# Optimization experiments

Hardware: AMD Instinct MI355X
Metric: run time of the kernel (lower is better)

Reference implementation:

```python
import jax, jax.numpy as jnp
import numpy as np

EPS_BN = 1e-5
NEG_SLOPE = 0.2

def gat_layer(x, src, dst, N, W, a_src, a_dst, b, heads, ch, concat):
    # x: [N, Fin]; W: [Fin, heads*ch]; a_src/a_dst: [heads, ch]; b: [heads*ch] or [ch]
    xw = (x @ W).reshape(N, heads, ch)                      # [N,H,C]
    al_src = jnp.einsum('nhc,hc->nh', xw, a_src)            # [N,H]
    al_dst = jnp.einsum('nhc,hc->nh', xw, a_dst)
    e = jax.nn.leaky_relu(al_src[src] + al_dst[dst], NEG_SLOPE)  # [E,H]
    m = jax.ops.segment_max(e, dst, num_segments=N)         # segment softmax (stable)
    ee = jnp.exp(e - m[dst])
    s = jax.ops.segment_sum(ee, dst, num_segments=N)
    alpha = ee / (s[dst] + 1e-16)                            # [E,H]
    msg = xw[src] * alpha[:, :, None]                        # [E,H,C]
    out = jax.ops.segment_sum(msg, dst, num_segments=N)      # [N,H,C]
    if concat:
        return out.reshape(N, heads * ch) + b
    return out.mean(axis=1) + b

def setup_inputs():
    key = jax.random.key(0)
    ks = jax.random.split(key, 24)
    N, E, dim_in, dim_out = 20000, 320000, 256, 16
    x = jax.random.normal(ks[0], (N, dim_in), dtype=jnp.float32)
    edge_index = jax.random.randint(ks[1], (2, E), 0, N, dtype=jnp.int64)
    def glorot(k, shape):
        fan = shape[0] + shape[-1]
        return jax.random.uniform(k, shape, jnp.float32, -1.0, 1.0) * np.sqrt(6.0 / fan)
    return {
        'x': x, 'edge_index': edge_index,
        'bn_gamma': jnp.ones((dim_in,), jnp.float32),
        'bn_beta': jnp.zeros((dim_in,), jnp.float32),
        'W1': glorot(ks[2], (dim_in, 16 * 64)),
        'a1_src': glorot(ks[3], (16, 64)), 'a1_dst': glorot(ks[4], (16, 64)),
        'b1': jnp.zeros((16 * 64,), jnp.float32),
        'p1': jnp.float32(0.25),
        'W2': glorot(ks[5], (dim_in + 16 * 64, 8 * 8)),
        'a2_src': glorot(ks[6], (8, 8)), 'a2_dst': glorot(ks[7], (8, 8)),
        'b2': jnp.zeros((8 * 8,), jnp.float32),
        'p2': jnp.float32(0.25),
        'W3': glorot(ks[8], (8 * 8, 8 * dim_out)),
        'a3_src': glorot(ks[9], (8, dim_out)), 'a3_dst': glorot(ks[10], (8, dim_out)),
        'b3': jnp.zeros((dim_out,), jnp.float32),
    }

def reference(x, edge_index, bn_gamma, bn_beta, W1, a1_src, a1_dst, b1, p1,
              W2, a2_src, a2_dst, b2, p2, W3, a3_src, a3_dst, b3):
    N = x.shape[0]
    # PyG GATConv default add_self_loops=True
    loops = jnp.arange(N, dtype=edge_index.dtype)
    src = jnp.concatenate([edge_index[0], loops])
    dst = jnp.concatenate([edge_index[1], loops])
    # BatchNorm1d (training-mode batch stats)
    mu = x.mean(axis=0)
    var = x.var(axis=0)
    x_in = (x - mu) * jax.lax.rsqrt(var + EPS_BN) * bn_gamma + bn_beta
    h = gat_layer(x_in, src, dst, N, W1, a1_src, a1_dst, b1, 16, 64, True)
    h = jnp.where(h >= 0, h, p1 * h)  # PReLU
    h = gat_layer(jnp.concatenate([x_in, h], axis=1), src, dst, N, W2, a2_src, a2_dst, b2, 8, 8, True)
    h = jnp.where(h >= 0, h, p2 * h)
    h = gat_layer(h, src, dst, N, W3, a3_src, a3_dst, b3, 8, b3.shape[0], False)
    return jax.nn.log_softmax(h, axis=1)
```

## Files before the change

### kernel.cpp

```cpp
#include <hip/hip_runtime.h>
#include <math.h>

typedef unsigned int u32;
typedef unsigned short u16;
typedef u32 u32x4 __attribute__((ext_vector_type(4)));
typedef float f32x4 __attribute__((ext_vector_type(4)));

__device__ __forceinline__ u16 f2bf(float f) {
  u32 u = __builtin_bit_cast(u32, f);
  return (u16)((u + 0x7FFFu + ((u >> 16) & 1u)) >> 16);
}
__device__ __forceinline__ float bf2f(u32 lo16) {
  return __builtin_bit_cast(float, lo16 << 16);
}
__device__ __forceinline__ void mfma16(f32x4& c, const u32x4& a, const u32x4& b) {
  asm volatile("v_mfma_f32_16x16x32_bf16 %0, %1, %2, %0" : "+v"(c) : "v"(a), "v"(b));
}
__device__ __forceinline__ float lrelu(float e) { return fmaxf(e, 0.2f * e); }

__global__ void bn_stats_kernel(const float* __restrict__ x, float* __restrict__ musum,
                                float* __restrict__ sqsum, int N, int F) {
  int t = threadIdx.x;
  float s = 0.f, s2 = 0.f;
  for (int r = blockIdx.x; r < N; r += gridDim.x) {
    float v = x[(size_t)r * F + t];
    s += v;
    s2 += v * v;
  }
  atomicAdd(&musum[t], s);
  atomicAdd(&sqsum[t], s2);
}

__global__ void bn_finalize_kernel(const float* __restrict__ musum, const float* __restrict__ sqsum,
                                   const float* __restrict__ gamma, const float* __restrict__ beta,
                                   float* __restrict__ scale, float* __restrict__ shift, int N) {
  int t = threadIdx.x;
  float m = musum[t] / (float)N;
  float v = sqsum[t] / (float)N - m * m;
  float sc = gamma[t] * rsqrtf(v + 1e-5f);
  scale[t] = sc;
  shift[t] = beta[t] - m * sc;
}

__global__ void bn_apply_bf16_kernel(const float* __restrict__ x, const float* __restrict__ scale,
                                     const float* __restrict__ shift, u16* __restrict__ xin,
                                     int total, int Fmask) {
  int i = blockIdx.x * blockDim.x + threadIdx.x;
  if (i < total) {
    int c = i & Fmask;
    xin[i] = f2bf(x[i] * scale[c] + shift[c]);
  }
}

__global__ void csr_count_kernel(const int* __restrict__ ei, int E, int N, int* __restrict__ cnt) {
  int e = blockIdx.x * blockDim.x + threadIdx.x;
  int ET = E + N;
  if (e < ET) {
    int d = (e < E) ? ei[E + e] : (e - E);
    atomicAdd(&cnt[d], 1);
  }
}

__global__ __launch_bounds__(1024) void csr_scan_kernel(const int* __restrict__ cnt,
                                                        int* __restrict__ row_ptr,
                                                        int* __restrict__ cursor, int N) {
  __shared__ int part[1024];
  int t = threadIdx.x;
  int chunk = (N + 1023) / 1024;
  int lo = t * chunk;
  int hi = min(lo + chunk, N);
  int s = 0;
  for (int i = lo; i < hi; i++) s += cnt[i];
  part[t] = s;
  __syncthreads();
  for (int off = 1; off < 1024; off <<= 1) {
    int v = (t >= off) ? part[t - off] : 0;
    __syncthreads();
    part[t] += v;
    __syncthreads();
  }
  int run = (t == 0) ? 0 : part[t - 1];
  for (int i = lo; i < hi; i++) {
    row_ptr[i] = run;
    cursor[i] = run;
    run += cnt[i];
  }
  if (t == 1023) row_ptr[N] = part[1023];
}

__global__ void csr_fill_kernel(const int* __restrict__ ei, int E, int N,
                                int* __restrict__ cursor, int* __restrict__ csr_src) {
  int e = blockIdx.x * blockDim.x + threadIdx.x;
  int ET = E + N;
  if (e < ET) {
    int s, d;
    if (e < E) { s = ei[e]; d = ei[E + e]; }
    else       { s = e - E; d = s; }
    int pos = atomicAdd(&cursor[d], 1);
    csr_src[pos] = s;
  }
}

__global__ __launch_bounds__(1024) void perm_build_kernel(const int* __restrict__ row_ptr,
                                                          int* __restrict__ perm, int N) {
  __shared__ int bins[256];
  __shared__ int base[256];
  int t = threadIdx.x;
  if (t < 256) bins[t] = 0;
  __syncthreads();
  for (int i = t; i < N; i += 1024) {
    int d = min(row_ptr[i + 1] - row_ptr[i], 255);
    atomicAdd(&bins[d], 1);
  }
  __syncthreads();
  for (int off = 1; off < 256; off <<= 1) {
    int u = (t < 256 && t >= off) ? bins[t - off] : 0;
    __syncthreads();
    if (t < 256) bins[t] += u;
    __syncthreads();
  }
  if (t < 256) base[t] = (t == 0) ? 0 : bins[t - 1];
  __syncthreads();
  if (t < 256) bins[t] = base[t];
  __syncthreads();
  for (int i = t; i < N; i += 1024) {
    int d = min(row_ptr[i + 1] - row_ptr[i], 255);
    int pos = atomicAdd(&bins[d], 1);
    perm[pos] = i;
  }
}

__global__ void wt_build_all(const float* __restrict__ W1, const float* __restrict__ W2,
                             const float* __restrict__ W3, u16* __restrict__ Wt1,
                             u16* __restrict__ Wt2, u16* __restrict__ Wt3) {
  const int S1 = 1024 * 256, S2 = 64 * 1280, S3 = 128 * 64;
  const int P1 = 96 * 256, P2 = 32 * 1280, P3 = 32 * 64;
  int idx = blockIdx.x * blockDim.x + threadIdx.x;
  if (idx < S1) {
    int n = idx / 256, k = idx % 256;
    Wt1[idx] = f2bf(W1[(size_t)k * 1024 + n]);
  } else if (idx < S1 + S2) {
    int i = idx - S1;
    int n = i / 1280, k = i % 1280;
    Wt2[i] = f2bf(W2[(size_t)k * 64 + n]);
  } else if (idx < S1 + S2 + S3) {
    int i = idx - S1 - S2;
    int n = i / 64, k = i % 64;
    Wt3[i] = f2bf(W3[(size_t)k * 128 + n]);
  } else if (idx < S1 + S2 + S3 + P1) {
    Wt1[S1 + (idx - S1 - S2 - S3)] = 0;
  } else if (idx < S1 + S2 + S3 + P1 + P2) {
    Wt2[S2 + (idx - S1 - S2 - S3 - P1)] = 0;
  } else if (idx < S1 + S2 + S3 + P1 + P2 + P3) {
    Wt3[S3 + (idx - S1 - S2 - S3 - P1 - P2)] = 0;
  }
}

__global__ void alfold_build(const float* __restrict__ W1, const float* __restrict__ a1s,
                             const float* __restrict__ a1d, const float* __restrict__ W2,
                             const float* __restrict__ a2s, const float* __restrict__ a2d,
                             const float* __restrict__ W3, const float* __restrict__ a3s,
                             const float* __restrict__ a3d, u16* __restrict__ Wt1,
                             u16* __restrict__ Wt2, u16* __restrict__ Wt3) {
  const int T1 = 32 * 256, T2 = 16 * 1280, T3 = 16 * 64;
  int idx = blockIdx.x * blockDim.x + threadIdx.x;
  if (idx < T1) {
    int jj = idx / 256, k = idx % 256, h = jj >> 1;
    const float* av = (jj & 1) ? a1d : a1s;
    float s = 0.f;
    for (int c = 0; c < 64; c++) s += W1[(size_t)k * 1024 + h * 64 + c] * av[h * 64 + c];
    Wt1[(size_t)(1024 + jj) * 256 + k] = f2bf(s);
  } else if (idx < T1 + T2) {
    int i = idx - T1;
    int jj = i / 1280, k = i % 1280, h = jj >> 1;
    const float* av = (jj & 1) ? a2d : a2s;
    float s = 0.f;
    for (int c = 0; c < 8; c++) s += W2[(size_t)k * 64 + h * 8 + c] * av[h * 8 + c];
    Wt2[(size_t)(64 + jj) * 1280 + k] = f2bf(s);
  } else if (idx < T1 + T2 + T3) {
    int i = idx - T1 - T2;
    int jj = i / 64, k = i % 64, h = jj >> 1;
    const float* av = (jj & 1) ? a3d : a3s;
    float s = 0.f;
    for (int c = 0; c < 16; c++) s += W3[(size_t)k * 128 + h * 16 + c] * av[h * 16 + c];
    Wt3[(size_t)(128 + jj) * 64 + k] = f2bf(s);
  }
}

template <int BM, int BN, int FM, int FN>
__global__ __launch_bounds__(256) void mfma_gemm_al(
    const u16* __restrict__ A1, const u16* __restrict__ A2, int K1, int K,
    const u16* __restrict__ Wt, u16* __restrict__ Ch, int NcH,
    float* __restrict__ als, float* __restrict__ ald, int ALN, int ALP, int M) {
  constexpr int BK = 32;
  constexpr int ACH = (BM * BK) / 8;
  constexpr int BCH = (BN * BK) / 8;
  static_assert(BM == 2 * FM * 16 && BN == 2 * FN * 16, "wave grid 2x2");
  __shared__ u16 As[BM * BK];
  __shared__ u16 Bs[BN * BK];
  int t = threadIdx.x;
  int m0 = blockIdx.x * BM, n0 = blockIdx.y * BN;
  int r = t & 15;
  int g = (t >> 4) & 3;
  int wid = t >> 6;
  int wm0 = (wid >> 1) * (FM * 16);
  int wn0 = (wid & 1) * (FN * 16);
  int K8 = K >> 3;
  int K2 = K - K1;

  f32x4 acc[FM][FN] = {};
  asm volatile("s_nop 7\n\ts_nop 7" :::);

  for (int k0 = 0; k0 < K; k0 += BK) {
    const u16* Aseg;
    int sA, kl;
    if (k0 < K1) { Aseg = A1; sA = K1; kl = k0; }
    else         { Aseg = A2; sA = K2; kl = k0 - K1; }
    __syncthreads();
#pragma unroll
    for (int i = 0; i < (ACH + 255) / 256; i++) {
      int c = i * 256 + t;
      if (ACH % 256 == 0 || c < ACH) {
        int m = c >> 2, kb = c & 3;
        *(u32x4*)(As + c * 8) =
            *(const u32x4*)(Aseg + (size_t)(m0 + m) * sA + kl + kb * 8);
      }
    }
#pragma unroll
    for (int i = 0; i < (BCH + 255) / 256; i++) {
      int c = i * 256 + t;
      if (BCH % 256 == 0 || c < BCH) {
        int nn = c >> 2, kb = c & 3;
        *(u32x4*)(Bs + c * 8) =
            *(const u32x4*)(Wt + ((size_t)(n0 + nn) * K8 + (k0 >> 3) + kb) * 8);
      }
    }
    __syncthreads();
    u32x4 af[FM], bfr[FN];
#pragma unroll
    for (int fi = 0; fi < FM; fi++)
      af[fi] = *(const u32x4*)(As + ((wm0 + fi * 16 + r) * 4 + g) * 8);
#pragma unroll
    for (int fj = 0; fj < FN; fj++)
      bfr[fj] = *(const u32x4*)(Bs + ((wn0 + fj * 16 + r) * 4 + g) * 8);
#pragma unroll
    for (int fi = 0; fi < FM; fi++)
#pragma unroll
      for (int fj = 0; fj < FN; fj++) mfma16(acc[fi][fj], af[fi], bfr[fj]);
  }
  asm volatile("s_nop 7\n\ts_nop 7" :::);

#pragma unroll
  for (int fi = 0; fi < FM; fi++) {
#pragma unroll
    for (int fj = 0; fj < FN; fj++) {
#pragma unroll
      for (int v = 0; v < 4; v++) {
        int m = m0 + wm0 + fi * 16 + g * 4 + v;
        int nn = n0 + wn0 + fj * 16 + r;
        if (m < M) {
          float val = acc[fi][fj][v];
          if (nn < NcH) {
            Ch[(size_t)m * NcH + nn] = f2bf(val);
          } else {
            int j = nn - NcH;
            if (j < ALN) ((j & 1) ? ald : als)[(size_t)(j >> 1) * ALP + m] = val;
          }
        }
      }
    }
  }
}

__global__ __launch_bounds__(256) void gat_agg1_gs(
    const u16* __restrict__ xwh, const float* __restrict__ alsrc,
    const float* __restrict__ aldst, const int* __restrict__ row_ptr,
    const int* __restrict__ csr_src, const int* __restrict__ perm,
    const float* __restrict__ bias, const float* __restrict__ slope_p,
    u16* __restrict__ out, int N, int ALP, int NBH) {
  constexpr int U = 4;
  int b = blockIdx.x;
  int xcd = b & 7, seq = b >> 3;
  int phase = seq / NBH, nb = seq - phase * NBH;
  int h = xcd + (phase << 3);
  int lane = threadIdx.x & 63;
  int g = lane >> 3, l8 = lane & 7;
  int ti = nb * 32 + (threadIdx.x >> 6) * 8 + g;
  int n = perm[min(ti, N - 1)];
  const float* alh = alsrc + (size_t)h * ALP;
  float ad = aldst[(size_t)h * ALP + n];
  int start = row_ptr[n];
  int end = row_ptr[n + 1];
  int deg = (ti < N) ? end - start : 0;
  int endm1 = end - 1;

  float m = -1e30f, s = 0.f;
  float acc[8] = {};
  const u16* base = xwh + (size_t)h * 64 + (size_t)l8 * 8;

  auto fma8 = [&](const u32x4& v, float w) {
#pragma unroll
    for (int i = 0; i < 4; i++) {
      u32 u = v[i];
      acc[2 * i] = fmaf(w, bf2f(u & 0xffffu), acc[2 * i]);
      acc[2 * i + 1] = fmaf(w, bf2f(u >> 16), acc[2 * i + 1]);
    }
  };

  int c[U];
#pragma unroll
  for (int i = 0; i < U; i++) c[i] = csr_src[min(start + i, endm1)];
  int j = 0;
  for (; j + U <= deg; j += U) {
    u32x4 v[U];
    float e[U];
#pragma unroll
    for (int i = 0; i < U; i++) v[i] = *(const u32x4*)(base + (size_t)c[i] * 1024);
#pragma unroll
    for (int i = 0; i < U; i++) e[i] = lrelu(alh[c[i]] + ad);
#pragma unroll
    for (int i = 0; i < U; i++) c[i] = csr_src[min(start + j + U + i, endm1)];
    float mn = fmaxf(fmaxf(e[0], e[1]), fmaxf(e[2], e[3]));
    if (mn > m) {
      float sc = __expf(m - mn);
      s *= sc;
#pragma unroll
      for (int k = 0; k < 8; k++) acc[k] *= sc;
      m = mn;
    }
#pragma unroll
    for (int i = 0; i < U; i++) {
      float w = __expf(e[i] - m);
      s += w;
      fma8(v[i], w);
    }
  }
  for (int i = 0; j < deg; j++, i++) {
    u32x4 v = *(const u32x4*)(base + (size_t)c[i] * 1024);
    float e = lrelu(alh[c[i]] + ad);
    if (e > m) {
      float sc = __expf(m - e);
      s *= sc;
#pragma unroll
      for (int k = 0; k < 8; k++) acc[k] *= sc;
      m = e;
    }
    float w = __expf(e - m);
    s += w;
    fma8(v, w);
  }
  float rr = 1.f / (s + 1e-16f);

  if (ti < N) {
    float p = slope_p[0];
    u32 ow[4];
#pragma unroll
    for (int i = 0; i < 4; i++) {
      int cc = h * 64 + l8 * 8 + 2 * i;
      float v0 = acc[2 * i] * rr + bias[cc];
      float v1 = acc[2 * i + 1] * rr + bias[cc + 1];
      v0 = (v0 >= 0.f) ? v0 : p * v0;
      v1 = (v1 >= 0.f) ? v1 : p * v1;
      ow[i] = (u32)f2bf(v0) | ((u32)f2bf(v1) << 16);
    }
    *(u32x4*)(out + (size_t)n * 1024 + h * 64 + l8 * 8) = *(u32x4*)ow;
  }
}

__global__ __launch_bounds__(256) void gat_agg2_wave(
    const u16* __restrict__ xwh, const float* __restrict__ alsrc,
    const float* __restrict__ aldst, const int* __restrict__ row_ptr,
    const int* __restrict__ csr_src, const float* __restrict__ bias,
    const float* __restrict__ slope_p, u16* __restrict__ out, int N, int ALP) {
  constexpr int U = 8;
  int n = blockIdx.x * 4 + (threadIdx.x >> 6);
  if (n >= N) return;
  int lane = threadIdx.x & 63;
  int head = lane >> 3;
  const float* alh = alsrc + (size_t)head * ALP;
  float ad = aldst[(size_t)head * ALP + n];
  int start = row_ptr[n];
  int end = row_ptr[n + 1];
  int deg = end - start;
  int endm1 = end - 1;

  float m = -1e30f, s = 0.f, acc = 0.f;
  int c[U];
#pragma unroll
  for (int i = 0; i < U; i++) c[i] = csr_src[min(start + i, endm1)];
  int j = 0;
  for (; j + U <= deg; j += U) {
    u16 v[U];
    float e[U];
#pragma unroll
    for (int i = 0; i < U; i++) v[i] = xwh[(size_t)c[i] * 64 + lane];
#pragma unroll
    for (int i = 0; i < U; i++) e[i] = lrelu(alh[c[i]] + ad);
#pragma unroll
    for (int i = 0; i < U; i++) c[i] = csr_src[min(start + j + U + i, endm1)];
    float mn = e[0];
#pragma unroll
    for (int i = 1; i < U; i++) mn = fmaxf(mn, e[i]);
    if (mn > m) {
      float sc = __expf(m - mn);
      s *= sc;
      acc *= sc;
      m = mn;
    }
#pragma unroll
    for (int i = 0; i < U; i++) {
      float w = __expf(e[i] - m);
      s += w;
      acc = fmaf(w, bf2f(v[i]), acc);
    }
  }
  for (int i = 0; j < deg; j++, i++) {
    float vv = bf2f(xwh[(size_t)c[i] * 64 + lane]);
    float e = lrelu(alh[c[i]] + ad);
    if (e > m) {
      float sc = __expf(m - e);
      s *= sc;
      acc *= sc;
      m = e;
    }
    float w = __expf(e - m);
    s += w;
    acc = fmaf(w, vv, acc);
  }
  float rr = 1.f / (s + 1e-16f);

  float p = slope_p[0];
  float v = acc * rr + bias[lane];
  out[(size_t)n * 64 + lane] = f2bf((v >= 0.f) ? v : p * v);
}

__global__ __launch_bounds__(256) void gat_agg3_wave(
    const u16* __restrict__ xwh, const float* __restrict__ alsrc,
    const float* __restrict__ aldst, const int* __restrict__ row_ptr,
    const int* __restrict__ csr_src, const float* __restrict__ bias,
    float* __restrict__ out, int N, int ALP) {
  constexpr int U = 8;
  int n = blockIdx.x * 4 + (threadIdx.x >> 6);
  if (n >= N) return;
  int lane = threadIdx.x & 63;
  int head = lane >> 3;
  const float* alh = alsrc + (size_t)head * ALP;
  float ad = aldst[(size_t)head * ALP + n];
  int start = row_ptr[n];
  int end = row_ptr[n + 1];
  int deg = end - start;
  int endm1 = end - 1;

  float m = -1e30f, s = 0.f, a0 = 0.f, a1 = 0.f;
  int c[U];
#pragma unroll
  for (int i = 0; i < U; i++) c[i] = csr_src[min(start + i, endm1)];
  int j = 0;
  for (; j + U <= deg; j += U) {
    u32 v[U];
    float e[U];
#pragma unroll
    for (int i = 0; i < U; i++) v[i] = *(const u32*)(xwh + (size_t)c[i] * 128 + lane * 2);
#pragma unroll
    for (int i = 0; i < U; i++) e[i] = lrelu(alh[c[i]] + ad);
#pragma unroll
    for (int i = 0; i < U; i++) c[i] = csr_src[min(start + j + U + i, endm1)];
    float mn = e[0];
#pragma unroll
    for (int i = 1; i < U; i++) mn = fmaxf(mn, e[i]);
    if (mn > m) {
      float sc = __expf(m - mn);
      s *= sc;
      a0 *= sc;
      a1 *= sc;
      m = mn;
    }
#pragma unroll
    for (int i = 0; i < U; i++) {
      float w = __expf(e[i] - m);
      s += w;
      a0 = fmaf(w, bf2f(v[i] & 0xffffu), a0);
      a1 = fmaf(w, bf2f(v[i] >> 16), a1);
    }
  }
  for (int i = 0; j < deg; j++, i++) {
    u32 v = *(const u32*)(xwh + (size_t)c[i] * 128 + lane * 2);
    float e = lrelu(alh[c[i]] + ad);
    if (e > m) {
      float sc = __expf(m - e);
      s *= sc;
      a0 *= sc;
      a1 *= sc;
      m = e;
    }
    float w = __expf(e - m);
    s += w;
    a0 = fmaf(w, bf2f(v & 0xffffu), a0);
    a1 = fmaf(w, bf2f(v >> 16), a1);
  }
  float rr = 1.f / (s + 1e-16f);
  a0 *= rr;
  a1 *= rr;

#pragma unroll
  for (int st = 8; st <= 32; st <<= 1) {
    a0 += __shfl_xor(a0, st);
    a1 += __shfl_xor(a1, st);
  }
  int c0 = (2 * lane) & 15, c1 = (2 * lane + 1) & 15;
  float v0 = a0 * 0.125f + bias[c0];
  float v1 = a1 * 0.125f + bias[c1];
  float mx = fmaxf(v0, v1);
#pragma unroll
  for (int st = 1; st <= 4; st <<= 1) mx = fmaxf(mx, __shfl_xor(mx, st));
  float se = __expf(v0 - mx) + __expf(v1 - mx);
#pragma unroll
  for (int st = 1; st <= 4; st <<= 1) se += __shfl_xor(se, st);
  float lse = mx + logf(se);
  if (lane < 8) {
    float2 o = make_float2(v0 - lse, v1 - lse);
    *((float2*)(out + (size_t)n * 16) + lane) = o;
  }
}

extern "C" void kernel_launch(void* const* d_in, const int* in_sizes, int n_in,
                              void* d_out, int out_size, void* d_ws, size_t ws_size,
                              hipStream_t stream) {
  const float* x        = (const float*)d_in[0];
  const int*   ei       = (const int*)d_in[1];
  const float* bn_gamma = (const float*)d_in[2];
  const float* bn_beta  = (const float*)d_in[3];
  const float* W1       = (const float*)d_in[4];
  const float* a1s      = (const float*)d_in[5];
  const float* a1d      = (const float*)d_in[6];
  const float* b1       = (const float*)d_in[7];
  const float* p1       = (const float*)d_in[8];
  const float* W2       = (const float*)d_in[9];
  const float* a2s      = (const float*)d_in[10];
  const float* a2d      = (const float*)d_in[11];
  const float* b2       = (const float*)d_in[12];
  const float* p2       = (const float*)d_in[13];
  const float* W3       = (const float*)d_in[14];
  const float* a3s      = (const float*)d_in[15];
  const float* a3d      = (const float*)d_in[16];
  const float* b3       = (const float*)d_in[17];
  float* out = (float*)d_out;

  const int F  = in_sizes[2];
  const int N  = in_sizes[0] / F;
  const int E  = in_sizes[1] / 2;
  const int ET = E + N;
  const int MP = ((N + 127) / 128) * 128;

  size_t off = 0;
  auto alloc = [&](size_t bytes) -> char* {
    char* r = (char*)d_ws + off;
    off += (bytes + 255) & ~(size_t)255;
    return r;
  };
  float* musum   = (float*)alloc(F * 4);
  float* sqsum   = (float*)alloc(F * 4);
  float* scale   = (float*)alloc(F * 4);
  float* shift   = (float*)alloc(F * 4);
  int*   row_ptr = (int*)alloc((size_t)(N + 1) * 4);
  int*   cursor  = (int*)alloc((size_t)N * 4);
  int*   csr_src = (int*)alloc((size_t)ET * 4);
  int*   perm    = (int*)alloc((size_t)N * 4);
  float* al_s    = (float*)alloc((size_t)16 * MP * 4);
  float* al_d    = (float*)alloc((size_t)16 * MP * 4);
  u16*   Wt1     = (u16*)alloc((size_t)1152 * 256 * 2);
  u16*   Wt2     = (u16*)alloc((size_t)96 * 1280 * 2);
  u16*   Wt3     = (u16*)alloc((size_t)160 * 64 * 2);
  u16*   x_in_h  = (u16*)alloc((size_t)MP * 256 * 2);
  u16*   xw1h    = (u16*)alloc((size_t)MP * 1024 * 2);
  u16*   h1      = (u16*)alloc((size_t)MP * 1024 * 2);
  u16*   xw2h    = (u16*)alloc((size_t)MP * 64 * 2);
  u16*   h2h     = (u16*)alloc((size_t)MP * 64 * 2);
  u16*   xw3h    = (u16*)alloc((size_t)MP * 128 * 2);

  hipMemsetAsync(musum, 0, (size_t)2 * F * 4, stream);
  bn_stats_kernel<<<256, 256, 0, stream>>>(x, musum, sqsum, N, F);
  bn_finalize_kernel<<<1, F, 0, stream>>>(musum, sqsum, bn_gamma, bn_beta, scale, shift, N);
  int totalXF = N * F;
  bn_apply_bf16_kernel<<<(totalXF + 255) / 256, 256, 0, stream>>>(x, scale, shift, x_in_h,
                                                                  totalXF, F - 1);

  hipMemsetAsync(cursor, 0, (size_t)N * 4, stream);
  csr_count_kernel<<<(ET + 255) / 256, 256, 0, stream>>>(ei, E, N, cursor);
  csr_scan_kernel<<<1, 1024, 0, stream>>>(cursor, row_ptr, cursor, N);
  csr_fill_kernel<<<(ET + 255) / 256, 256, 0, stream>>>(ei, E, N, cursor, csr_src);

  perm_build_kernel<<<1, 1024, 0, stream>>>(row_ptr, perm, N);

  {
    int total = 1024 * 256 + 64 * 1280 + 128 * 64 + 96 * 256 + 32 * 1280 + 32 * 64;
    wt_build_all<<<(total + 255) / 256, 256, 0, stream>>>(W1, W2, W3, Wt1, Wt2, Wt3);
    int tot2 = 32 * 256 + 16 * 1280 + 16 * 64;
    alfold_build<<<(tot2 + 255) / 256, 256, 0, stream>>>(W1, a1s, a1d, W2, a2s, a2d, W3, a3s, a3d,
                                                         Wt1, Wt2, Wt3);
  }

  int nblk = (N + 3) / 4;

  {
    dim3 grid(MP / 128, 9);
    mfma_gemm_al<128, 128, 4, 4><<<grid, 256, 0, stream>>>(
        x_in_h, x_in_h, 256, 256, Wt1, xw1h, 1024, al_s, al_d, 32, MP, N);
    int NBH = (N + 31) / 32;
    gat_agg1_gs<<<8 * NBH * 2, 256, 0, stream>>>(xw1h, al_s, al_d, row_ptr, csr_src, perm, b1, p1,
                                                 h1, N, MP, NBH);
  }

  {
    dim3 grid((N + 63) / 64, 1);
    mfma_gemm_al<64, 96, 2, 3><<<grid, 256, 0, stream>>>(
        x_in_h, h1, 256, 1280, Wt2, xw2h, 64, al_s, al_d, 16, MP, N);
    gat_agg2_wave<<<nblk, 256, 0, stream>>>(xw2h, al_s, al_d, row_ptr, csr_src, b2, p2, h2h, N, MP);
  }

  {
    dim3 grid((N + 63) / 64, 1);
    mfma_gemm_al<64, 160, 2, 5><<<grid, 256, 0, stream>>>(
        h2h, h2h, 64, 64, Wt3, xw3h, 128, al_s, al_d, 16, MP, N);
    gat_agg3_wave<<<nblk, 256, 0, stream>>>(xw3h, al_s, al_d, row_ptr, csr_src, b3, out, N, MP);
  }
}
```

Baseline: 327.1 us.

## Double-buffer GEMM with direct global-to-LDS loads; regroup layer 2/3 aggregation lanes

```diff
diff --git a/kernel.cpp b/kernel.cpp
--- a/kernel.cpp
+++ b/kernel.cpp
@@ -196,8 +196,8 @@
   constexpr int ACH = (BM * BK) / 8;
   constexpr int BCH = (BN * BK) / 8;
   static_assert(BM == 2 * FM * 16 && BN == 2 * FN * 16, "wave grid 2x2");
-  __shared__ u16 As[BM * BK];
-  __shared__ u16 Bs[BN * BK];
+  __shared__ u16 As[2][BM * BK];
+  __shared__ u16 Bs[2][BN * BK];
   int t = threadIdx.x;
   int m0 = blockIdx.x * BM, n0 = blockIdx.y * BN;
   int r = t & 15;
@@ -208,22 +208,19 @@
   int K8 = K >> 3;
   int K2 = K - K1;
 
-  f32x4 acc[FM][FN] = {};
-  asm volatile("s_nop 7\n\ts_nop 7" :::);
-
-  for (int k0 = 0; k0 < K; k0 += BK) {
+  auto stage = [&](int buf, int k0) {
     const u16* Aseg;
     int sA, kl;
     if (k0 < K1) { Aseg = A1; sA = K1; kl = k0; }
     else         { Aseg = A2; sA = K2; kl = k0 - K1; }
-    __syncthreads();
 #pragma unroll
     for (int i = 0; i < (ACH + 255) / 256; i++) {
       int c = i * 256 + t;
       if (ACH % 256 == 0 || c < ACH) {
         int m = c >> 2, kb = c & 3;
-        *(u32x4*)(As + c * 8) =
-            *(const u32x4*)(Aseg + (size_t)(m0 + m) * sA + kl + kb * 8);
+        __builtin_amdgcn_global_load_lds(
+            (const __attribute__((address_space(1))) void*)(Aseg + (size_t)(m0 + m) * sA + kl + kb * 8),
+            (__attribute__((address_space(3))) void*)(&As[buf][c * 8]), 16, 0, 0);
       }
     }
 #pragma unroll
@@ -231,22 +228,34 @@
       int c = i * 256 + t;
       if (BCH % 256 == 0 || c < BCH) {
         int nn = c >> 2, kb = c & 3;
-        *(u32x4*)(Bs + c * 8) =
-            *(const u32x4*)(Wt + ((size_t)(n0 + nn) * K8 + (k0 >> 3) + kb) * 8);
+        __builtin_amdgcn_global_load_lds(
+            (const __attribute__((address_space(1))) void*)(Wt + ((size_t)(n0 + nn) * K8 + (k0 >> 3) + kb) * 8),
+            (__attribute__((address_space(3))) void*)(&Bs[buf][c * 8]), 16, 0, 0);
       }
     }
+  };
+
+  f32x4 acc[FM][FN] = {};
+  asm volatile("s_nop 7\n\ts_nop 7" :::);
+
+  stage(0, 0);
+  __syncthreads();
+  int nt = K / BK;
+  for (int ts = 0; ts < nt; ts++) {
+    if (ts + 1 < nt) stage((ts + 1) & 1, (ts + 1) * BK);
+    int cur = ts & 1;
+    u32x4 af[FM], bfr[FN];
+#pragma unroll
+    for (int fi = 0; fi < FM; fi++)
+      af[fi] = *(const u32x4*)(&As[cur][((wm0 + fi * 16 + r) * 4 + g) * 8]);
+#pragma unroll
+    for (int fj = 0; fj < FN; fj++)
+      bfr[fj] = *(const u32x4*)(&Bs[cur][((wn0 + fj * 16 + r) * 4 + g) * 8]);
+#pragma unroll
+    for (int fi = 0; fi < FM; fi++)
+#pragma unroll
+      for (int fj = 0; fj < FN; fj++) mfma16(acc[fi][fj], af[fi], bfr[fj]);
     __syncthreads();
-    u32x4 af[FM], bfr[FN];
-#pragma unroll
-    for (int fi = 0; fi < FM; fi++)
-      af[fi] = *(const u32x4*)(As + ((wm0 + fi * 16 + r) * 4 + g) * 8);
-#pragma unroll
-    for (int fj = 0; fj < FN; fj++)
-      bfr[fj] = *(const u32x4*)(Bs + ((wn0 + fj * 16 + r) * 4 + g) * 8);
-#pragma unroll
-    for (int fi = 0; fi < FM; fi++)
-#pragma unroll
-      for (int fj = 0; fj < FN; fj++) mfma16(acc[fi][fj], af[fi], bfr[fj]);
   }
   asm volatile("s_nop 7\n\ts_nop 7" :::);
 
@@ -367,159 +376,199 @@
   }
 }
 
-__global__ __launch_bounds__(256) void gat_agg2_wave(
+__global__ __launch_bounds__(256) void gat_agg2_gs(
     const u16* __restrict__ xwh, const float* __restrict__ alsrc,
     const float* __restrict__ aldst, const int* __restrict__ row_ptr,
-    const int* __restrict__ csr_src, const float* __restrict__ bias,
-    const float* __restrict__ slope_p, u16* __restrict__ out, int N, int ALP) {
-  constexpr int U = 8;
-  int n = blockIdx.x * 4 + (threadIdx.x >> 6);
-  if (n >= N) return;
+    const int* __restrict__ csr_src, const int* __restrict__ perm,
+    const float* __restrict__ bias, const float* __restrict__ slope_p,
+    u16* __restrict__ out, int N, int ALP) {
+  constexpr int U = 4;
   int lane = threadIdx.x & 63;
-  int head = lane >> 3;
+  int g = lane >> 3, l8 = lane & 7;
+  int ti = blockIdx.x * 32 + (threadIdx.x >> 6) * 8 + g;
+  int n = perm[min(ti, N - 1)];
+  const float* alh = alsrc + (size_t)l8 * ALP;
+  float ad = aldst[(size_t)l8 * ALP + n];
+  int start = row_ptr[n];
+  int end = row_ptr[n + 1];
+  int deg = (ti < N) ? end - start : 0;
+  int endm1 = end - 1;
+
+  float m = -1e30f, s = 0.f;
+  float acc[8] = {};
+  const u16* base = xwh + (size_t)l8 * 8;
+
+  auto fma8 = [&](const u32x4& v, float w) {
+#pragma unroll
+    for (int i = 0; i < 4; i++) {
+      u32 u = v[i];
+      acc[2 * i] = fmaf(w, bf2f(u & 0xffffu), acc[2 * i]);
+      acc[2 * i + 1] = fmaf(w, bf2f(u >> 16), acc[2 * i + 1]);
+    }
+  };
+
+  int c[U];
+#pragma unroll
+  for (int i = 0; i < U; i++) c[i] = csr_src[min(start + i, endm1)];
+  int j = 0;
+  for (; j + U <= deg; j += U) {
+    u32x4 v[U];
+    float e[U];
+#pragma unroll
+    for (int i = 0; i < U; i++) v[i] = *(const u32x4*)(base + (size_t)c[i] * 64);
+#pragma unroll
+    for (int i = 0; i < U; i++) e[i] = lrelu(alh[c[i]] + ad);
+#pragma unroll
+    for (int i = 0; i < U; i++) c[i] = csr_src[min(start + j + U + i, endm1)];
+    float mn = fmaxf(fmaxf(e[0], e[1]), fmaxf(e[2], e[3]));
+    if (mn > m) {
+      float sc = __expf(m - mn);
+      s *= sc;
+#pragma unroll
+      for (int k = 0; k < 8; k++) acc[k] *= sc;
+      m = mn;
+    }
+#pragma unroll
+    for (int i = 0; i < U; i++) {
+      float w = __expf(e[i] - m);
+      s += w;
+      fma8(v[i], w);
+    }
+  }
+  for (int i = 0; j < deg; j++, i++) {
+    u32x4 v = *(const u32x4*)(base + (size_t)c[i] * 64);
+    float e = lrelu(alh[c[i]] + ad);
+    if (e > m) {
+      float sc = __expf(m - e);
+      s *= sc;
+#pragma unroll
+      for (int k = 0; k < 8; k++) acc[k] *= sc;
+      m = e;
+    }
+    float w = __expf(e - m);
+    s += w;
+    fma8(v, w);
+  }
+  float rr = 1.f / (s + 1e-16f);
+
+  if (ti < N) {
+    float p = slope_p[0];
+    u32 ow[4];
+#pragma unroll
+    for (int i = 0; i < 4; i++) {
+      int cc = l8 * 8 + 2 * i;
+      float v0 = acc[2 * i] * rr + bias[cc];
+      float v1 = acc[2 * i + 1] * rr + bias[cc + 1];
+      v0 = (v0 >= 0.f) ? v0 : p * v0;
+      v1 = (v1 >= 0.f) ? v1 : p * v1;
+      ow[i] = (u32)f2bf(v0) | ((u32)f2bf(v1) << 16);
+    }
+    *(u32x4*)(out + (size_t)n * 64 + l8 * 8) = *(u32x4*)ow;
+  }
+}
+
+__global__ __launch_bounds__(256) void gat_agg3_gs(
+    const u16* __restrict__ xwh, const float* __restrict__ alsrc,
+    const float* __restrict__ aldst, const int* __restrict__ row_ptr,
+    const int* __restrict__ csr_src, const int* __restrict__ perm,
+    const float* __restrict__ bias, float* __restrict__ out, int N, int ALP) {
+  constexpr int U = 4;
+  int lane = threadIdx.x & 63;
+  int g = lane >> 4, l16 = lane & 15;
+  int head = l16 >> 1;
+  int ti = blockIdx.x * 16 + (threadIdx.x >> 6) * 4 + g;
+  int n = perm[min(ti, N - 1)];
   const float* alh = alsrc + (size_t)head * ALP;
   float ad = aldst[(size_t)head * ALP + n];
   int start = row_ptr[n];
   int end = row_ptr[n + 1];
-  int deg = end - start;
+  int deg = (ti < N) ? end - start : 0;
   int endm1 = end - 1;
 
-  float m = -1e30f, s = 0.f, acc = 0.f;
+  float m = -1e30f, s = 0.f;
+  float acc[8] = {};
+  const u16* base = xwh + (size_t)l16 * 8;
+
+  auto fma8 = [&](const u32x4& v, float w) {
+#pragma unroll
+    for (int i = 0; i < 4; i++) {
+      u32 u = v[i];
+      acc[2 * i] = fmaf(w, bf2f(u & 0xffffu), acc[2 * i]);
+      acc[2 * i + 1] = fmaf(w, bf2f(u >> 16), acc[2 * i + 1]);
+    }
+  };
+
   int c[U];
 #pragma unroll
   for (int i = 0; i < U; i++) c[i] = csr_src[min(start + i, endm1)];
   int j = 0;
   for (; j + U <= deg; j += U) {
-    u16 v[U];
+    u32x4 v[U];
     float e[U];
 #pragma unroll
-    for (int i = 0; i < U; i++) v[i] = xwh[(size_t)c[i] * 64 + lane];
+    for (int i = 0; i < U; i++) v[i] = *(const u32x4*)(base + (size_t)c[i] * 128);
 #pragma unroll
     for (int i = 0; i < U; i++) e[i] = lrelu(alh[c[i]] + ad);
 #pragma unroll
     for (int i = 0; i < U; i++) c[i] = csr_src[min(start + j + U + i, endm1)];
-    float mn = e[0];
-#pragma unroll
-    for (int i = 1; i < U; i++) mn = fmaxf(mn, e[i]);
+    float mn = fmaxf(fmaxf(e[0], e[1]), fmaxf(e[2], e[3]));
     if (mn > m) {
       float sc = __expf(m - mn);
       s *= sc;
-      acc *= sc;
+#pragma unroll
+      for (int k = 0; k < 8; k++) acc[k] *= sc;
       m = mn;
     }
 #pragma unroll
     for (int i = 0; i < U; i++) {
       float w = __expf(e[i] - m);
       s += w;
-      acc = fmaf(w, bf2f(v[i]), acc);
+      fma8(v[i], w);
     }
   }
   for (int i = 0; j < deg; j++, i++) {
-    float vv = bf2f(xwh[(size_t)c[i] * 64 + lane]);
+    u32x4 v = *(const u32x4*)(base + (size_t)c[i] * 128);
     float e = lrelu(alh[c[i]] + ad);
     if (e > m) {
       float sc = __expf(m - e);
       s *= sc;
-      acc *= sc;
+#pragma unroll
+      for (int k = 0; k < 8; k++) acc[k] *= sc;
       m = e;
     }
     float w = __expf(e - m);
     s += w;
-    acc = fmaf(w, vv, acc);
+    fma8(v, w);
   }
   float rr = 1.f / (s + 1e-16f);
-
-  float p = slope_p[0];
-  float v = acc * rr + bias[lane];
-  out[(size_t)n * 64 + lane] = f2bf((v >= 0.f) ? v : p * v);
-}
-
-__global__ __launch_bounds__(256) void gat_agg3_wave(
-    const u16* __restrict__ xwh, const float* __restrict__ alsrc,
-    const float* __restrict__ aldst, const int* __restrict__ row_ptr,
-    const int* __restrict__ csr_src, const float* __restrict__ bias,
-    float* __restrict__ out, int N, int ALP) {
-  constexpr int U = 8;
-  int n = blockIdx.x * 4 + (threadIdx.x >> 6);
-  if (n >= N) return;
-  int lane = threadIdx.x & 63;
-  int head = lane >> 3;
-  const float* alh = alsrc + (size_t)head * ALP;
-  float ad = aldst[(size_t)head * ALP + n];
-  int start = row_ptr[n];
-  int end = row_ptr[n + 1];
-  int deg = end - start;
-  int endm1 = end - 1;
-
-  float m = -1e30f, s = 0.f, a0 = 0.f, a1 = 0.f;
-  int c[U];
-#pragma unroll
-  for (int i = 0; i < U; i++) c[i] = csr_src[min(start + i, endm1)];
-  int j = 0;
-  for (; j + U <= deg; j += U) {
-    u32 v[U];
-    float e[U];
-#pragma unroll
-    for (int i = 0; i < U; i++) v[i] = *(const u32*)(xwh + (size_t)c[i] * 128 + lane * 2);
-#pragma unroll
-    for (int i = 0; i < U; i++) e[i] = lrelu(alh[c[i]] + ad);
-#pragma unroll
-    for (int i = 0; i < U; i++) c[i] = csr_src[min(start + j + U + i, endm1)];
-    float mn = e[0];
-#pragma unroll
-    for (int i = 1; i < U; i++) mn = fmaxf(mn, e[i]);
-    if (mn > m) {
-      float sc = __expf(m - mn);
-      s *= sc;
-      a0 *= sc;
-      a1 *= sc;
-      m = mn;
-    }
-#pragma unroll
-    for (int i = 0; i < U; i++) {
-      float w = __expf(e[i] - m);
-      s += w;
-      a0 = fmaf(w, bf2f(v[i] & 0xffffu), a0);
-      a1 = fmaf(w, bf2f(v[i] >> 16), a1);
-    }
-  }
-  for (int i = 0; j < deg; j++, i++) {
-    u32 v = *(const u32*)(xwh + (size_t)c[i] * 128 + lane * 2);
-    float e = lrelu(alh[c[i]] + ad);
-    if (e > m) {
-      float sc = __expf(m - e);
-      s *= sc;
-      a0 *= sc;
-      a1 *= sc;
-      m = e;
-    }
-    float w = __expf(e - m);
-    s += w;
-    a0 = fmaf(w, bf2f(v & 0xffffu), a0);
-    a1 = fmaf(w, bf2f(v >> 16), a1);
-  }
-  float rr = 1.f / (s + 1e-16f);
-  a0 *= rr;
-  a1 *= rr;
-
-#pragma unroll
-  for (int st = 8; st <= 32; st <<= 1) {
-    a0 += __shfl_xor(a0, st);
-    a1 += __shfl_xor(a1, st);
-  }
-  int c0 = (2 * lane) & 15, c1 = (2 * lane + 1) & 15;
-  float v0 = a0 * 0.125f + bias[c0];
-  float v1 = a1 * 0.125f + bias[c1];
-  float mx = fmaxf(v0, v1);
-#pragma unroll
-  for (int st = 1; st <= 4; st <<= 1) mx = fmaxf(mx, __shfl_xor(mx, st));
-  float se = __expf(v0 - mx) + __expf(v1 - mx);
-#pragma unroll
-  for (int st = 1; st <= 4; st <<= 1) se += __shfl_xor(se, st);
+#pragma unroll
+  for (int k = 0; k < 8; k++) acc[k] *= rr;
+
+#pragma unroll
+  for (int st = 2; st <= 8; st <<= 1)
+#pragma unroll
+    for (int k = 0; k < 8; k++) acc[k] += __shfl_xor(acc[k], st);
+
+  int half = l16 & 1;
+  float v8[8];
+  float mx = -1e30f;
+#pragma unroll
+  for (int k = 0; k < 8; k++) {
+    v8[k] = acc[k] * 0.125f + bias[half * 8 + k];
+    mx = fmaxf(mx, v8[k]);
+  }
+  mx = fmaxf(mx, __shfl_xor(mx, 1));
+  float se = 0.f;
+#pragma unroll
+  for (int k = 0; k < 8; k++) se += __expf(v8[k] - mx);
+  se += __shfl_xor(se, 1);
   float lse = mx + logf(se);
-  if (lane < 8) {
-    float2 o = make_float2(v0 - lse, v1 - lse);
-    *((float2*)(out + (size_t)n * 16) + lane) = o;
+  if (ti < N && l16 < 2) {
+    float4 o0 = make_float4(v8[0] - lse, v8[1] - lse, v8[2] - lse, v8[3] - lse);
+    float4 o1 = make_float4(v8[4] - lse, v8[5] - lse, v8[6] - lse, v8[7] - lse);
+    float* op = out + (size_t)n * 16 + half * 8;
+    *(float4*)op = o0;
+    *(float4*)(op + 4) = o1;
   }
 }
 
@@ -600,8 +649,6 @@
                                                          Wt1, Wt2, Wt3);
   }
 
-  int nblk = (N + 3) / 4;
-
   {
     dim3 grid(MP / 128, 9);
     mfma_gemm_al<128, 128, 4, 4><<<grid, 256, 0, stream>>>(
@@ -615,13 +662,15 @@
     dim3 grid((N + 63) / 64, 1);
     mfma_gemm_al<64, 96, 2, 3><<<grid, 256, 0, stream>>>(
         x_in_h, h1, 256, 1280, Wt2, xw2h, 64, al_s, al_d, 16, MP, N);
-    gat_agg2_wave<<<nblk, 256, 0, stream>>>(xw2h, al_s, al_d, row_ptr, csr_src, b2, p2, h2h, N, MP);
+    gat_agg2_gs<<<(N + 31) / 32, 256, 0, stream>>>(xw2h, al_s, al_d, row_ptr, csr_src, perm, b2,
+                                                   p2, h2h, N, MP);
   }
 
   {
     dim3 grid((N + 63) / 64, 1);
     mfma_gemm_al<64, 160, 2, 5><<<grid, 256, 0, stream>>>(
         h2h, h2h, 64, 64, Wt3, xw3h, 128, al_s, al_d, 16, MP, N);
-    gat_agg3_wave<<<nblk, 256, 0, stream>>>(xw3h, al_s, al_d, row_ptr, csr_src, b3, out, N, MP);
-  }
-}
+    gat_agg3_gs<<<(N + 15) / 16, 256, 0, stream>>>(xw3h, al_s, al_d, row_ptr, csr_src, perm, b3,
+                                                   out, N, MP);
+  }
+}
```

Result: faster. 316.3 us (-3.3%).
